# Optimization experiments

Measured on AMD Instinct MI355X. Metric: run time of the kernel, lower is better.

The kernel has to match this reference:

```python
import jax, jax.numpy as jnp
import numpy as np

N = 8192
IN_F = 512
OUT_F = 256
ALPHA = 0.2


def setup_inputs() -> dict:
    key = jax.random.key(0)
    k1, k2, k3 = jax.random.split(key, 3)
    inp = jax.random.normal(k1, (N, IN_F), dtype=jnp.float32)
    # xavier_uniform with gain=1.414
    def xavier(k, shape, gain=1.414):
        fan_in, fan_out = shape[0], shape[1]
        bound = gain * np.sqrt(6.0 / (fan_in + fan_out))
        return jax.random.uniform(k, shape, jnp.float32, -bound, bound)
    W = xavier(k2, (IN_F, OUT_F))
    a = xavier(k3, (2 * OUT_F, 1))
    adj = jnp.ones((N, N), dtype=jnp.int32)  # unused by the original forward
    return {"input": inp, "adj": adj, "W": W, "a": a}


def reference(input, adj, W, a):
    # h: [N, F]
    h = input @ W
    F_ = h.shape[1]
    # Original builds [N, N, 2F] pairwise concat then matmul with a [2F,1].
    # Equivalent: e[i,j] = leaky_relu(h[i] . a[:F] + h[j] . a[F:])
    src = h @ a[:F_, 0]   # [N]
    dst = h @ a[F_:, 0]   # [N]
    e = jax.nn.leaky_relu(src[:, None] + dst[None, :], negative_slope=ALPHA)  # [N, N]
    attention = jax.nn.softmax(e, axis=1)  # adj is NOT applied in original code
    h_prime = attention @ h  # [N, F]
    return jax.nn.elu(h_prime)
```

## Files before the change

### kernel.cpp

```cpp
#include <hip/hip_runtime.h>
#include <math.h>

#define NR 8192
#define INF_ 512
#define OUTF 256
#define ALPHA 0.2f

__global__ __launch_bounds__(256) void k_gemm(const float* __restrict__ A,
                                              const float* __restrict__ W,
                                              float* __restrict__ H) {
    __shared__ float As[16][68];
    __shared__ float Bs[16][68];
    const int tid = threadIdx.x;
    const int brow = blockIdx.x * 64;
    const int bcol = blockIdx.y * 64;
    const int tx = tid & 15, ty = tid >> 4;
    const int ar = tid >> 2;
    const int ac = (tid & 3) << 2;
    const int br = tid >> 4;
    const int bc = (tid & 15) << 2;

    float acc[4][4] = {};
    for (int k0 = 0; k0 < INF_; k0 += 16) {
        float4 av = *(const float4*)(A + (size_t)(brow + ar) * INF_ + k0 + ac);
        float4 bv = *(const float4*)(W + (size_t)(k0 + br) * OUTF + bcol + bc);
        __syncthreads();
        As[ac + 0][ar] = av.x; As[ac + 1][ar] = av.y;
        As[ac + 2][ar] = av.z; As[ac + 3][ar] = av.w;
        *(float4*)&Bs[br][bc] = bv;
        __syncthreads();
#pragma unroll
        for (int kk = 0; kk < 16; ++kk) {
            float4 a4 = *(const float4*)&As[kk][ty * 4];
            float4 b4 = *(const float4*)&Bs[kk][tx * 4];
            acc[0][0] = fmaf(a4.x, b4.x, acc[0][0]); acc[0][1] = fmaf(a4.x, b4.y, acc[0][1]);
            acc[0][2] = fmaf(a4.x, b4.z, acc[0][2]); acc[0][3] = fmaf(a4.x, b4.w, acc[0][3]);
            acc[1][0] = fmaf(a4.y, b4.x, acc[1][0]); acc[1][1] = fmaf(a4.y, b4.y, acc[1][1]);
            acc[1][2] = fmaf(a4.y, b4.z, acc[1][2]); acc[1][3] = fmaf(a4.y, b4.w, acc[1][3]);
            acc[2][0] = fmaf(a4.z, b4.x, acc[2][0]); acc[2][1] = fmaf(a4.z, b4.y, acc[2][1]);
            acc[2][2] = fmaf(a4.z, b4.z, acc[2][2]); acc[2][3] = fmaf(a4.z, b4.w, acc[2][3]);
            acc[3][0] = fmaf(a4.w, b4.x, acc[3][0]); acc[3][1] = fmaf(a4.w, b4.y, acc[3][1]);
            acc[3][2] = fmaf(a4.w, b4.z, acc[3][2]); acc[3][3] = fmaf(a4.w, b4.w, acc[3][3]);
        }
    }
#pragma unroll
    for (int m = 0; m < 4; ++m) {
        float4 o = make_float4(acc[m][0], acc[m][1], acc[m][2], acc[m][3]);
        *(float4*)(H + (size_t)(brow + ty * 4 + m) * OUTF + bcol + tx * 4) = o;
    }
}

__global__ __launch_bounds__(256) void k_srcdst(const float* __restrict__ H,
                                                const float* __restrict__ a,
                                                float* __restrict__ src,
                                                float* __restrict__ dst) {
    const int wv = threadIdx.x >> 6;
    const int ln = threadIdx.x & 63;
    const int row = blockIdx.x * 4 + wv;
    float4 hv = *(const float4*)(H + (size_t)row * OUTF + ln * 4);
    float4 a1 = *(const float4*)(a + ln * 4);
    float4 a2 = *(const float4*)(a + OUTF + ln * 4);
    float s = hv.x * a1.x + hv.y * a1.y + hv.z * a1.z + hv.w * a1.w;
    float d = hv.x * a2.x + hv.y * a2.y + hv.z * a2.z + hv.w * a2.w;
#pragma unroll
    for (int o = 32; o > 0; o >>= 1) {
        s += __shfl_down(s, o);
        d += __shfl_down(d, o);
    }
    if (ln == 0) { src[row] = s; dst[row] = d; }
}

__global__ __launch_bounds__(256) void k_rank(const float* __restrict__ dstv,
                                              float* __restrict__ dsts,
                                              int* __restrict__ perm) {
    __shared__ float key[NR];
    const int tid = threadIdx.x;
#pragma unroll
    for (int i = 0; i < 8; ++i)
        *(float4*)(key + 4 * (tid + 256 * i)) = *(const float4*)(dstv + 4 * (tid + 256 * i));
    __syncthreads();
    const int el = blockIdx.x * 32 + (tid >> 3);
    const int sub = tid & 7;
    const float my = key[el];
    const int sbase = sub << 10;
    int cnt = 0;
#pragma unroll 4
    for (int i = 0; i < 256; ++i) {
        const int off = ((i + sub) << 2) & 1023;
        const int k0 = sbase + off;
        float4 v = *(const float4*)(key + k0);
        cnt += (int)((v.x < my) | ((v.x == my) & (k0 + 0 < el)));
        cnt += (int)((v.y < my) | ((v.y == my) & (k0 + 1 < el)));
        cnt += (int)((v.z < my) | ((v.z == my) & (k0 + 2 < el)));
        cnt += (int)((v.w < my) | ((v.w == my) & (k0 + 3 < el)));
    }
    cnt += __shfl_down(cnt, 4);
    cnt += __shfl_down(cnt, 2);
    cnt += __shfl_down(cnt, 1);
    if (sub == 0) {
        dsts[cnt] = my;
        perm[cnt] = el;
    }
}

__global__ __launch_bounds__(1024) void k_scan(const float* __restrict__ dsts,
                                               float* __restrict__ wplus,
                                               float* __restrict__ wminus,
                                               float* __restrict__ Splus,
                                               float* __restrict__ Sminus) {
    __shared__ float wsP[16], wsM[16];
    const int t = threadIdx.x;
    const int lane = t & 63;
    const float D = dsts[NR - 1];
    float4 v0 = *(const float4*)(dsts + t * 8);
    float4 v1 = *(const float4*)(dsts + t * 8 + 4);
    float vv[8] = {v0.x, v0.y, v0.z, v0.w, v1.x, v1.y, v1.z, v1.w};
    float wp[8], wm[8];
    float sp = 0.f, sm = 0.f;
#pragma unroll
    for (int j = 0; j < 8; ++j) {
        wp[j] = expf(vv[j] - D);
        wm[j] = expf(ALPHA * vv[j]);
        sp += wp[j]; sm += wm[j];
    }
    *(float4*)(wplus + t * 8)      = make_float4(wp[0], wp[1], wp[2], wp[3]);
    *(float4*)(wplus + t * 8 + 4)  = make_float4(wp[4], wp[5], wp[6], wp[7]);
    *(float4*)(wminus + t * 8)     = make_float4(wm[0], wm[1], wm[2], wm[3]);
    *(float4*)(wminus + t * 8 + 4) = make_float4(wm[4], wm[5], wm[6], wm[7]);
    float ip = sp, im = sm;
#pragma unroll
    for (int o = 1; o < 64; o <<= 1) {
        float tp = __shfl_up(ip, o);
        float tm = __shfl_up(im, o);
        if (lane >= o) { ip += tp; im += tm; }
    }
    if (lane == 63) { wsP[t >> 6] = ip; wsM[t >> 6] = im; }
    __syncthreads();
    if (t < 16) {
        float a = wsP[t], b = wsM[t];
#pragma unroll
        for (int o = 1; o < 16; o <<= 1) {
            float ta = __shfl_up(a, o);
            float tb = __shfl_up(b, o);
            if (t >= o) { a += ta; b += tb; }
        }
        wsP[t] = a; wsM[t] = b;
    }
    __syncthreads();
    const int w = t >> 6;
    float rp = (w ? wsP[w - 1] : 0.f) + (ip - sp);
    float rm = (w ? wsM[w - 1] : 0.f) + (im - sm);
#pragma unroll
    for (int j = 0; j < 8; ++j) {
        rp += wp[j]; rm += wm[j];
        Splus[t * 8 + j + 1] = rp;
        Sminus[t * 8 + j + 1] = rm;
    }
    if (t == 0) { Splus[0] = 0.f; Sminus[0] = 0.f; }
}

__global__ __launch_bounds__(256) void k_chunksum(const float* __restrict__ H,
                                                  const int* __restrict__ perm,
                                                  const float* __restrict__ wplus,
                                                  const float* __restrict__ wminus,
                                                  float* __restrict__ chunkP,
                                                  float* __restrict__ chunkM) {
    const int b = blockIdx.x, f = threadIdx.x;
    float aP = 0.f, aM = 0.f;
#pragma unroll 4
    for (int k = 0; k < 32; ++k) {
        int g = b * 32 + k;
        int p = perm[g];
        float hv = H[(size_t)p * OUTF + f];
        aP = fmaf(wplus[g], hv, aP);
        aM = fmaf(wminus[g], hv, aM);
    }
    chunkP[b * OUTF + f] = aP;
    chunkM[b * OUTF + f] = aM;
}

__global__ __launch_bounds__(64) void k_chunkscan(const float* __restrict__ chunkP,
                                                  const float* __restrict__ chunkM,
                                                  float* __restrict__ offP,
                                                  float* __restrict__ offM,
                                                  float* __restrict__ PrefP,
                                                  float* __restrict__ PrefM) {
    const int f = blockIdx.x;
    const bool minus = (blockIdx.y != 0);
    const float* sv = minus ? chunkM : chunkP;
    float* dv = minus ? offM : offP;
    float* tot = minus ? PrefM : PrefP;
    const int l = threadIdx.x;
    float v0 = sv[(4 * l + 0) * OUTF + f];
    float v1 = sv[(4 * l + 1) * OUTF + f];
    float v2 = sv[(4 * l + 2) * OUTF + f];
    float v3 = sv[(4 * l + 3) * OUTF + f];
    float s = v0 + v1 + v2 + v3;
    float incl = s;
#pragma unroll
    for (int o = 1; o < 64; o <<= 1) {
        float t = __shfl_up(incl, o);
        if (l >= o) incl += t;
    }
    float excl = incl - s;
    dv[(4 * l + 0) * OUTF + f] = excl;
    dv[(4 * l + 1) * OUTF + f] = excl + v0;
    dv[(4 * l + 2) * OUTF + f] = excl + v0 + v1;
    dv[(4 * l + 3) * OUTF + f] = excl + v0 + v1 + v2;
    if (l == 63) tot[(size_t)NR * OUTF + f] = incl;
}

__global__ __launch_bounds__(256) void k_writepref(const float* __restrict__ H,
                                                   const int* __restrict__ perm,
                                                   const float* __restrict__ wplus,
                                                   const float* __restrict__ wminus,
                                                   const float* __restrict__ offP,
                                                   const float* __restrict__ offM,
                                                   float* __restrict__ PrefP,
                                                   float* __restrict__ PrefM) {
    const int b = blockIdx.x, f = threadIdx.x;
    float aP = offP[b * OUTF + f];
    float aM = offM[b * OUTF + f];
    for (int k = 0; k < 32; ++k) {
        int g = b * 32 + k;
        PrefP[(size_t)g * OUTF + f] = aP;
        PrefM[(size_t)g * OUTF + f] = aM;
        int p = perm[g];
        float hv = H[(size_t)p * OUTF + f];
        aP = fmaf(wplus[g], hv, aP);
        aM = fmaf(wminus[g], hv, aM);
    }
}

__global__ __launch_bounds__(256) void k_out(const float* __restrict__ src,
                                             const float* __restrict__ dsts,
                                             const float* __restrict__ Splus,
                                             const float* __restrict__ Sminus,
                                             const float* __restrict__ PrefP,
                                             const float* __restrict__ PrefM,
                                             float* __restrict__ out) {
    const int i = blockIdx.x, f = threadIdx.x;
    const float si = src[i];
    const float D = dsts[NR - 1];
    const float thr = -si;
    int lo = 0, hi = NR;
    while (lo < hi) {
        int mid = (lo + hi) >> 1;
        if (dsts[mid] <= thr) lo = mid + 1; else hi = mid;
    }
    const int t = lo;
    const float cP = expf(si + D);
    const float cM = expf(ALPHA * si);
    const float SP = Splus[NR] - Splus[t];
    const float SM = Sminus[t];
    const float inv = 1.f / (cP * SP + cM * SM);
    const float pP = PrefP[(size_t)NR * OUTF + f] - PrefP[(size_t)t * OUTF + f];
    const float pM = PrefM[(size_t)t * OUTF + f];
    const float v = (cP * pP + cM * pM) * inv;
    out[(size_t)i * OUTF + f] = v > 0.f ? v : expm1f(v);
}

extern "C" void kernel_launch(void* const* d_in, const int* in_sizes, int n_in,
                              void* d_out, int out_size, void* d_ws, size_t ws_size,
                              hipStream_t stream) {
    const float* X = (const float*)d_in[0];
    const float* W = (const float*)d_in[2];
    const float* a = (const float*)d_in[3];
    float* out = (float*)d_out;

    char* ws = (char*)d_ws;
    size_t off = 0;
    auto carve = [&](size_t bytes) -> void* {
        void* p = ws + off;
        off += (bytes + 1023) & ~(size_t)1023;
        return p;
    };
    float* H      = (float*)carve((size_t)NR * OUTF * 4);
    float* src    = (float*)carve(NR * 4);
    float* dstv   = (float*)carve(NR * 4);
    float* dsts   = (float*)carve(NR * 4);
    int*   perm   = (int*)carve(NR * 4);
    float* wplus  = (float*)carve(NR * 4);
    float* wminus = (float*)carve(NR * 4);
    float* Splus  = (float*)carve((NR + 1) * 4);
    float* Sminus = (float*)carve((NR + 1) * 4);
    float* chunkP = (float*)carve(256 * OUTF * 4);
    float* chunkM = (float*)carve(256 * OUTF * 4);
    float* offP   = (float*)carve(256 * OUTF * 4);
    float* offM   = (float*)carve(256 * OUTF * 4);
    float* PrefP  = (float*)carve((size_t)(NR + 1) * OUTF * 4);
    float* PrefM  = (float*)carve((size_t)(NR + 1) * OUTF * 4);

    k_gemm<<<dim3(NR / 64, OUTF / 64), 256, 0, stream>>>(X, W, H);
    k_srcdst<<<NR / 4, 256, 0, stream>>>(H, a, src, dstv);
    k_rank<<<NR / 32, 256, 0, stream>>>(dstv, dsts, perm);
    k_scan<<<1, 1024, 0, stream>>>(dsts, wplus, wminus, Splus, Sminus);
    k_chunksum<<<256, 256, 0, stream>>>(H, perm, wplus, wminus, chunkP, chunkM);
    k_chunkscan<<<dim3(OUTF, 2), 64, 0, stream>>>(chunkP, chunkM, offP, offM, PrefP, PrefM);
    k_writepref<<<256, 256, 0, stream>>>(H, perm, wplus, wminus, offP, offM, PrefP, PrefM);
    k_out<<<NR, 256, 0, stream>>>(src, dsts, Splus, Sminus, PrefP, PrefM, out);
}
```

Baseline: 444.4 us.

## Use split-bf16 MFMA for input projection and batch gathers in prefix kernels

The fp32 SIMT GEMM computing H = X·W is replaced by bf16 MFMA instructions that use a hi/lo split (three MFMAs per tile) to keep close to fp32 accuracy. This needs two new conversion kernels that write bf16 hi/lo copies of X and a transposed W. The GEMM register-prefetches the next K slice while the current one is computed. Separately, the chunksum and writepref kernels now stage perm and weights in shared memory, batch eight gathered H loads at a time, and double the block count. The cost is extra launches and extra memory traffic for the converted copies, plus a small loss of precision from the split-bf16 scheme.

```diff
diff --git a/kernel.cpp b/kernel.cpp
--- a/kernel.cpp
+++ b/kernel.cpp
@@ -6,47 +6,119 @@
 #define OUTF 256
 #define ALPHA 0.2f
 
-__global__ __launch_bounds__(256) void k_gemm(const float* __restrict__ A,
-                                              const float* __restrict__ W,
+typedef __attribute__((ext_vector_type(8))) short bf16x8;
+typedef __attribute__((ext_vector_type(4))) float f32x4;
+
+#define MFMA(a, b, c) __builtin_amdgcn_mfma_f32_16x16x32_bf16((a), (b), (c), 0, 0, 0)
+
+__device__ __forceinline__ ushort f2bf(float x) {
+    unsigned u = __float_as_uint(x);
+    unsigned r = (u + 0x7fff + ((u >> 16) & 1)) >> 16;
+    return (ushort)r;
+}
+__device__ __forceinline__ float bf2f(ushort b) { return __uint_as_float((unsigned)b << 16); }
+
+__global__ __launch_bounds__(256) void k_convX(const float* __restrict__ X,
+                                               ushort* __restrict__ Xhi,
+                                               ushort* __restrict__ Xlo) {
+    const size_t i = ((size_t)blockIdx.x * 256 + threadIdx.x) * 8;
+    float4 v0 = *(const float4*)(X + i);
+    float4 v1 = *(const float4*)(X + i + 4);
+    float f[8] = {v0.x, v0.y, v0.z, v0.w, v1.x, v1.y, v1.z, v1.w};
+    ushort hi[8], lo[8];
+#pragma unroll
+    for (int j = 0; j < 8; ++j) {
+        hi[j] = f2bf(f[j]);
+        lo[j] = f2bf(f[j] - bf2f(hi[j]));
+    }
+    *(uint4*)(Xhi + i) = *(uint4*)hi;
+    *(uint4*)(Xlo + i) = *(uint4*)lo;
+}
+
+__global__ __launch_bounds__(128) void k_convWT(const float* __restrict__ W,
+                                                ushort* __restrict__ Wthi,
+                                                ushort* __restrict__ Wtlo) {
+    const int c = blockIdx.x;
+    const int t = threadIdx.x;
+    ushort h[4], l[4];
+#pragma unroll
+    for (int j = 0; j < 4; ++j) {
+        float x = W[(size_t)(4 * t + j) * OUTF + c];
+        h[j] = f2bf(x);
+        l[j] = f2bf(x - bf2f(h[j]));
+    }
+    *(ushort4*)(Wthi + (size_t)c * INF_ + 4 * t) = *(ushort4*)h;
+    *(ushort4*)(Wtlo + (size_t)c * INF_ + 4 * t) = *(ushort4*)l;
+}
+
+__global__ __launch_bounds__(256) void k_gemm(const ushort* __restrict__ Xhi,
+                                              const ushort* __restrict__ Xlo,
+                                              const ushort* __restrict__ Wthi,
+                                              const ushort* __restrict__ Wtlo,
                                               float* __restrict__ H) {
-    __shared__ float As[16][68];
-    __shared__ float Bs[16][68];
+    __shared__ ushort sAhi[2048], sAlo[2048], sBhi[2048], sBlo[2048];
     const int tid = threadIdx.x;
     const int brow = blockIdx.x * 64;
     const int bcol = blockIdx.y * 64;
-    const int tx = tid & 15, ty = tid >> 4;
-    const int ar = tid >> 2;
-    const int ac = (tid & 3) << 2;
-    const int br = tid >> 4;
-    const int bc = (tid & 15) << 2;
-
-    float acc[4][4] = {};
-    for (int k0 = 0; k0 < INF_; k0 += 16) {
-        float4 av = *(const float4*)(A + (size_t)(brow + ar) * INF_ + k0 + ac);
-        float4 bv = *(const float4*)(W + (size_t)(k0 + br) * OUTF + bcol + bc);
+    const int lane = tid & 63;
+    const int wr = tid >> 6;
+    const int s_kg = tid >> 6, s_i = tid & 63;
+    const ushort* gAhi = Xhi + (size_t)(brow + s_i) * INF_ + s_kg * 8;
+    const ushort* gAlo = Xlo + (size_t)(brow + s_i) * INF_ + s_kg * 8;
+    const ushort* gBhi = Wthi + (size_t)(bcol + s_i) * INF_ + s_kg * 8;
+    const ushort* gBlo = Wtlo + (size_t)(bcol + s_i) * INF_ + s_kg * 8;
+    const int sw = tid * 8;
+
+    const int fr = lane & 15, kg = lane >> 4;
+    const int aoff = kg * 512 + (wr * 16 + fr) * 8;
+    const int boff = kg * 512 + fr * 8;
+
+    f32x4 acc0 = {0.f, 0.f, 0.f, 0.f};
+    f32x4 acc1 = {0.f, 0.f, 0.f, 0.f};
+    f32x4 acc2 = {0.f, 0.f, 0.f, 0.f};
+    f32x4 acc3 = {0.f, 0.f, 0.f, 0.f};
+
+    uint4 rAh = *(const uint4*)gAhi;
+    uint4 rAl = *(const uint4*)gAlo;
+    uint4 rBh = *(const uint4*)gBhi;
+    uint4 rBl = *(const uint4*)gBlo;
+
+    for (int t = 0; t < INF_ / 32; ++t) {
+        *(uint4*)&sAhi[sw] = rAh;
+        *(uint4*)&sAlo[sw] = rAl;
+        *(uint4*)&sBhi[sw] = rBh;
+        *(uint4*)&sBlo[sw] = rBl;
         __syncthreads();
-        As[ac + 0][ar] = av.x; As[ac + 1][ar] = av.y;
-        As[ac + 2][ar] = av.z; As[ac + 3][ar] = av.w;
-        *(float4*)&Bs[br][bc] = bv;
+        if (t < INF_ / 32 - 1) {
+            rAh = *(const uint4*)(gAhi + (t + 1) * 32);
+            rAl = *(const uint4*)(gAlo + (t + 1) * 32);
+            rBh = *(const uint4*)(gBhi + (t + 1) * 32);
+            rBl = *(const uint4*)(gBlo + (t + 1) * 32);
+        }
+        bf16x8 ahi = *(const bf16x8*)&sAhi[aoff];
+        bf16x8 alo = *(const bf16x8*)&sAlo[aoff];
+        bf16x8 bh0 = *(const bf16x8*)&sBhi[boff];
+        bf16x8 bl0 = *(const bf16x8*)&sBlo[boff];
+        bf16x8 bh1 = *(const bf16x8*)&sBhi[boff + 128];
+        bf16x8 bl1 = *(const bf16x8*)&sBlo[boff + 128];
+        bf16x8 bh2 = *(const bf16x8*)&sBhi[boff + 256];
+        bf16x8 bl2 = *(const bf16x8*)&sBlo[boff + 256];
+        bf16x8 bh3 = *(const bf16x8*)&sBhi[boff + 384];
+        bf16x8 bl3 = *(const bf16x8*)&sBlo[boff + 384];
+        acc0 = MFMA(ahi, bh0, acc0); acc0 = MFMA(ahi, bl0, acc0); acc0 = MFMA(alo, bh0, acc0);
+        acc1 = MFMA(ahi, bh1, acc1); acc1 = MFMA(ahi, bl1, acc1); acc1 = MFMA(alo, bh1, acc1);
+        acc2 = MFMA(ahi, bh2, acc2); acc2 = MFMA(ahi, bl2, acc2); acc2 = MFMA(alo, bh2, acc2);
+        acc3 = MFMA(ahi, bh3, acc3); acc3 = MFMA(ahi, bl3, acc3); acc3 = MFMA(alo, bh3, acc3);
         __syncthreads();
-#pragma unroll
-        for (int kk = 0; kk < 16; ++kk) {
-            float4 a4 = *(const float4*)&As[kk][ty * 4];
-            float4 b4 = *(const float4*)&Bs[kk][tx * 4];
-            acc[0][0] = fmaf(a4.x, b4.x, acc[0][0]); acc[0][1] = fmaf(a4.x, b4.y, acc[0][1]);
-            acc[0][2] = fmaf(a4.x, b4.z, acc[0][2]); acc[0][3] = fmaf(a4.x, b4.w, acc[0][3]);
-            acc[1][0] = fmaf(a4.y, b4.x, acc[1][0]); acc[1][1] = fmaf(a4.y, b4.y, acc[1][1]);
-            acc[1][2] = fmaf(a4.y, b4.z, acc[1][2]); acc[1][3] = fmaf(a4.y, b4.w, acc[1][3]);
-            acc[2][0] = fmaf(a4.z, b4.x, acc[2][0]); acc[2][1] = fmaf(a4.z, b4.y, acc[2][1]);
-            acc[2][2] = fmaf(a4.z, b4.z, acc[2][2]); acc[2][3] = fmaf(a4.z, b4.w, acc[2][3]);
-            acc[3][0] = fmaf(a4.w, b4.x, acc[3][0]); acc[3][1] = fmaf(a4.w, b4.y, acc[3][1]);
-            acc[3][2] = fmaf(a4.w, b4.z, acc[3][2]); acc[3][3] = fmaf(a4.w, b4.w, acc[3][3]);
-        }
-    }
-#pragma unroll
-    for (int m = 0; m < 4; ++m) {
-        float4 o = make_float4(acc[m][0], acc[m][1], acc[m][2], acc[m][3]);
-        *(float4*)(H + (size_t)(brow + ty * 4 + m) * OUTF + bcol + tx * 4) = o;
+    }
+    const int orow = brow + wr * 16 + kg * 4;
+    const int ocol = bcol + fr;
+#pragma unroll
+    for (int q = 0; q < 4; ++q) {
+        H[(size_t)(orow + q) * OUTF + ocol + 0]  = acc0[q];
+        H[(size_t)(orow + q) * OUTF + ocol + 16] = acc1[q];
+        H[(size_t)(orow + q) * OUTF + ocol + 32] = acc2[q];
+        H[(size_t)(orow + q) * OUTF + ocol + 48] = acc3[q];
     }
 }
 
@@ -159,21 +231,33 @@
     if (t == 0) { Splus[0] = 0.f; Sminus[0] = 0.f; }
 }
 
-__global__ __launch_bounds__(256) void k_chunksum(const float* __restrict__ H,
+__global__ __launch_bounds__(128) void k_chunksum(const float* __restrict__ H,
                                                   const int* __restrict__ perm,
                                                   const float* __restrict__ wplus,
                                                   const float* __restrict__ wminus,
                                                   float* __restrict__ chunkP,
                                                   float* __restrict__ chunkM) {
-    const int b = blockIdx.x, f = threadIdx.x;
+    __shared__ int sp[32];
+    __shared__ float swp[32], swm[32];
+    const int b = blockIdx.x >> 1;
+    const int f = (blockIdx.x & 1) * 128 + threadIdx.x;
+    if (threadIdx.x < 32) {
+        int g = b * 32 + threadIdx.x;
+        sp[threadIdx.x] = perm[g];
+        swp[threadIdx.x] = wplus[g];
+        swm[threadIdx.x] = wminus[g];
+    }
+    __syncthreads();
     float aP = 0.f, aM = 0.f;
-#pragma unroll 4
-    for (int k = 0; k < 32; ++k) {
-        int g = b * 32 + k;
-        int p = perm[g];
-        float hv = H[(size_t)p * OUTF + f];
-        aP = fmaf(wplus[g], hv, aP);
-        aM = fmaf(wminus[g], hv, aM);
+    for (int k0 = 0; k0 < 32; k0 += 8) {
+        float hv[8];
+#pragma unroll
+        for (int j = 0; j < 8; ++j) hv[j] = H[(size_t)sp[k0 + j] * OUTF + f];
+#pragma unroll
+        for (int j = 0; j < 8; ++j) {
+            aP = fmaf(swp[k0 + j], hv[j], aP);
+            aM = fmaf(swm[k0 + j], hv[j], aM);
+        }
     }
     chunkP[b * OUTF + f] = aP;
     chunkM[b * OUTF + f] = aM;
@@ -210,7 +294,7 @@
     if (l == 63) tot[(size_t)NR * OUTF + f] = incl;
 }
 
-__global__ __launch_bounds__(256) void k_writepref(const float* __restrict__ H,
+__global__ __launch_bounds__(128) void k_writepref(const float* __restrict__ H,
                                                    const int* __restrict__ perm,
                                                    const float* __restrict__ wplus,
                                                    const float* __restrict__ wminus,
@@ -218,17 +302,31 @@
                                                    const float* __restrict__ offM,
                                                    float* __restrict__ PrefP,
                                                    float* __restrict__ PrefM) {
-    const int b = blockIdx.x, f = threadIdx.x;
+    __shared__ int sp[32];
+    __shared__ float swp[32], swm[32];
+    const int b = blockIdx.x >> 1;
+    const int f = (blockIdx.x & 1) * 128 + threadIdx.x;
+    if (threadIdx.x < 32) {
+        int g = b * 32 + threadIdx.x;
+        sp[threadIdx.x] = perm[g];
+        swp[threadIdx.x] = wplus[g];
+        swm[threadIdx.x] = wminus[g];
+    }
+    __syncthreads();
     float aP = offP[b * OUTF + f];
     float aM = offM[b * OUTF + f];
-    for (int k = 0; k < 32; ++k) {
-        int g = b * 32 + k;
-        PrefP[(size_t)g * OUTF + f] = aP;
-        PrefM[(size_t)g * OUTF + f] = aM;
-        int p = perm[g];
-        float hv = H[(size_t)p * OUTF + f];
-        aP = fmaf(wplus[g], hv, aP);
-        aM = fmaf(wminus[g], hv, aM);
+    for (int k0 = 0; k0 < 32; k0 += 8) {
+        float hv[8];
+#pragma unroll
+        for (int j = 0; j < 8; ++j) hv[j] = H[(size_t)sp[k0 + j] * OUTF + f];
+#pragma unroll
+        for (int j = 0; j < 8; ++j) {
+            int g = b * 32 + k0 + j;
+            PrefP[(size_t)g * OUTF + f] = aP;
+            PrefM[(size_t)g * OUTF + f] = aM;
+            aP = fmaf(swp[k0 + j], hv[j], aP);
+            aM = fmaf(swm[k0 + j], hv[j], aM);
+        }
     }
 }
 
@@ -275,28 +373,34 @@
         off += (bytes + 1023) & ~(size_t)1023;
         return p;
     };
-    float* H      = (float*)carve((size_t)NR * OUTF * 4);
-    float* src    = (float*)carve(NR * 4);
-    float* dstv   = (float*)carve(NR * 4);
-    float* dsts   = (float*)carve(NR * 4);
-    int*   perm   = (int*)carve(NR * 4);
-    float* wplus  = (float*)carve(NR * 4);
-    float* wminus = (float*)carve(NR * 4);
-    float* Splus  = (float*)carve((NR + 1) * 4);
-    float* Sminus = (float*)carve((NR + 1) * 4);
-    float* chunkP = (float*)carve(256 * OUTF * 4);
-    float* chunkM = (float*)carve(256 * OUTF * 4);
-    float* offP   = (float*)carve(256 * OUTF * 4);
-    float* offM   = (float*)carve(256 * OUTF * 4);
-    float* PrefP  = (float*)carve((size_t)(NR + 1) * OUTF * 4);
-    float* PrefM  = (float*)carve((size_t)(NR + 1) * OUTF * 4);
-
-    k_gemm<<<dim3(NR / 64, OUTF / 64), 256, 0, stream>>>(X, W, H);
+    float*  H      = (float*)carve((size_t)NR * OUTF * 4);
+    ushort* Xhi    = (ushort*)carve((size_t)NR * INF_ * 2);
+    ushort* Xlo    = (ushort*)carve((size_t)NR * INF_ * 2);
+    ushort* Wthi   = (ushort*)carve((size_t)OUTF * INF_ * 2);
+    ushort* Wtlo   = (ushort*)carve((size_t)OUTF * INF_ * 2);
+    float*  src    = (float*)carve(NR * 4);
+    float*  dstv   = (float*)carve(NR * 4);
+    float*  dsts   = (float*)carve(NR * 4);
+    int*    perm   = (int*)carve(NR * 4);
+    float*  wplus  = (float*)carve(NR * 4);
+    float*  wminus = (float*)carve(NR * 4);
+    float*  Splus  = (float*)carve((NR + 1) * 4);
+    float*  Sminus = (float*)carve((NR + 1) * 4);
+    float*  chunkP = (float*)carve(256 * OUTF * 4);
+    float*  chunkM = (float*)carve(256 * OUTF * 4);
+    float*  offP   = (float*)carve(256 * OUTF * 4);
+    float*  offM   = (float*)carve(256 * OUTF * 4);
+    float*  PrefP  = (float*)carve((size_t)(NR + 1) * OUTF * 4);
+    float*  PrefM  = (float*)carve((size_t)(NR + 1) * OUTF * 4);
+
+    k_convX<<<NR * INF_ / (256 * 8), 256, 0, stream>>>(X, Xhi, Xlo);
+    k_convWT<<<OUTF, 128, 0, stream>>>(W, Wthi, Wtlo);
+    k_gemm<<<dim3(NR / 64, OUTF / 64), 256, 0, stream>>>(Xhi, Xlo, Wthi, Wtlo, H);
     k_srcdst<<<NR / 4, 256, 0, stream>>>(H, a, src, dstv);
     k_rank<<<NR / 32, 256, 0, stream>>>(dstv, dsts, perm);
     k_scan<<<1, 1024, 0, stream>>>(dsts, wplus, wminus, Splus, Sminus);
-    k_chunksum<<<256, 256, 0, stream>>>(H, perm, wplus, wminus, chunkP, chunkM);
+    k_chunksum<<<512, 128, 0, stream>>>(H, perm, wplus, wminus, chunkP, chunkM);
     k_chunkscan<<<dim3(OUTF, 2), 64, 0, stream>>>(chunkP, chunkM, offP, offM, PrefP, PrefM);
-    k_writepref<<<256, 256, 0, stream>>>(H, perm, wplus, wminus, offP, offM, PrefP, PrefM);
+    k_writepref<<<512, 128, 0, stream>>>(H, perm, wplus, wminus, offP, offM, PrefP, PrefM);
     k_out<<<NR, 256, 0, stream>>>(src, dsts, Splus, Sminus, PrefP, PrefM, out);
 }
```

Measured after the change: 435.6 us. 2.0% less time.
